# Optimization experiments

Hardware: AMD Instinct MI355X
Metric: run time of the kernel (lower is better)

Reference implementation:

```python
import jax, jax.numpy as jnp
import numpy as np

B, S, H, NH, L, NS = 8, 4096, 768, 12, 2, 64
DH = H // NH
EPS = 1e-12


def _layer_norm(x, g, b):
    mu = jnp.mean(x, axis=-1, keepdims=True)
    var = jnp.mean((x - mu) ** 2, axis=-1, keepdims=True)
    return (x - mu) / jnp.sqrt(var + EPS) * g + b


def setup_inputs() -> dict:
    key = jax.random.key(0)
    ks = jax.random.split(key, 8)
    # sentence index per token: 64 equal contiguous sentences; position 0 is [CLS] in sentence 0
    sent_ind = jnp.broadcast_to((jnp.arange(S, dtype=jnp.int32) * NS) // S, (B, S)).astype(jnp.int32)
    start_layer = jax.random.normal(ks[0], (B, S, H), dtype=jnp.float32)
    init = lambda k, shape: (jax.random.normal(k, shape, dtype=jnp.float32) * 0.02)
    return {
        "sent_ind": sent_ind,
        "start_layer": start_layer,
        "Wq": init(ks[1], (L, H, H)), "bq": jnp.zeros((L, H), jnp.float32),
        "Wk": init(ks[2], (L, H, H)), "bk": jnp.zeros((L, H), jnp.float32),
        "Wv": init(ks[3], (L, H, H)), "bv": jnp.zeros((L, H), jnp.float32),
        "Wo": init(ks[4], (L, H, H)), "bo": jnp.zeros((L, H), jnp.float32),
        "ln_g": jnp.ones((L, H), jnp.float32), "ln_b": jnp.zeros((L, H), jnp.float32),
    }


def reference(sent_ind, start_layer, Wq, bq, Wk, bk, Wv, bv, Wo, bo, ln_g, ln_b):
    # ---- segment-mean pooling by sentence index (vectorized replacement of the python loops) ----
    onehot = (sent_ind[..., None] == jnp.arange(NS, dtype=sent_ind.dtype)).astype(start_layer.dtype)  # [B,S,NS]
    # the first [CLS] token is excluded from sentence 0's mean
    onehot = onehot.at[:, 0, :].set(0.0)
    sums = jnp.einsum('bsn,bsd->bnd', onehot, start_layer)          # [B,NS,H]
    counts = jnp.sum(onehot, axis=1)                                 # [B,NS]
    x = sums / counts[..., None]                                     # graph_vectors [B,NS,H]

    # ---- GAT layers: BertSelfAttention + GATSelfOutput(dense->gelu->LayerNorm), dropout=eval ----
    scale = 1.0 / (DH ** 0.5)
    for i in range(L):
        q = (x @ Wq[i] + bq[i]).reshape(B, NS, NH, DH)
        k = (x @ Wk[i] + bk[i]).reshape(B, NS, NH, DH)
        v = (x @ Wv[i] + bv[i]).reshape(B, NS, NH, DH)
        scores = jnp.einsum('bqhd,bkhd->bhqk', q, k) * scale
        probs = jax.nn.softmax(scores, axis=-1)
        ctx = jnp.einsum('bhqk,bkhd->bqhd', probs, v).reshape(B, NS, H)
        h = jax.nn.gelu(ctx @ Wo[i] + bo[i], approximate=False)
        x = _layer_norm(h, ln_g[i], ln_b[i])
    return x
```

## Files before the change

kernel.cpp:

```cpp
#include <hip/hip_runtime.h>
#include <hip/hip_bf16.h>

constexpr int cB  = 8;
constexpr int cS  = 4096;
constexpr int cH  = 768;
constexpr int cNH = 12;
constexpr int cL  = 2;
constexpr int cNS = 64;
constexpr int cDH = 64;
constexpr int cM  = cB * cNS;

typedef __attribute__((ext_vector_type(8))) short bf16x8;
typedef __attribute__((ext_vector_type(4))) float f32x4;

__global__ __launch_bounds__(256) void pool_kernel(
    const int* __restrict__ sent_ind, const float* __restrict__ sl,
    __hip_bfloat16* __restrict__ xb)
{
    int bn = blockIdx.x;
    int b = bn >> 6, n = bn & (cNS - 1);
    __shared__ int cnt;
    __shared__ int list[cS];
    if (threadIdx.x == 0) cnt = 0;
    __syncthreads();
    const int* si = sent_ind + (size_t)b * cS;
    for (int s = threadIdx.x; s < cS; s += 256)
        if (s != 0 && si[s] == n) { int p = atomicAdd(&cnt, 1); list[p] = s; }
    __syncthreads();
    int c = cnt;
    float a0 = 0.f, a1 = 0.f, a2 = 0.f;
    for (int i = 0; i < c; ++i) {
        const float* row = sl + ((size_t)b * cS + list[i]) * cH;
        a0 += row[threadIdx.x];
        a1 += row[threadIdx.x + 256];
        a2 += row[threadIdx.x + 512];
    }
    float inv = 1.0f / (float)c;
    __hip_bfloat16* xr = xb + (size_t)bn * cH;
    xr[threadIdx.x]       = __float2bfloat16(a0 * inv);
    xr[threadIdx.x + 256] = __float2bfloat16(a1 * inv);
    xr[threadIdx.x + 512] = __float2bfloat16(a2 * inv);
}

__global__ __launch_bounds__(256) void wconv_kernel(
    const float* __restrict__ Wq, const float* __restrict__ Wk,
    const float* __restrict__ Wv, const float* __restrict__ Wo,
    __hip_bfloat16* __restrict__ wt)
{
    int mat = blockIdx.z;
    int layer = mat >> 2, which = mat & 3;
    const float* W = (which == 0 ? Wq : which == 1 ? Wk : which == 2 ? Wv : Wo)
                     + (size_t)layer * cH * cH;
    __shared__ float T[64][65];
    int k0 = blockIdx.y * 64, n0 = blockIdx.x * 64;
    int tid = threadIdx.x;
    int r = tid >> 2, cb = (tid & 3) * 16;
    #pragma unroll
    for (int u = 0; u < 4; ++u) {
        float4 w4 = *(const float4*)(W + (size_t)(k0 + r) * cH + n0 + cb + u * 4);
        T[r][cb + u * 4 + 0] = w4.x; T[r][cb + u * 4 + 1] = w4.y;
        T[r][cb + u * 4 + 2] = w4.z; T[r][cb + u * 4 + 3] = w4.w;
    }
    __syncthreads();
    int kk = tid & 63;
    int nb = (tid >> 6) * 16;
    __hip_bfloat16* dst = wt + ((size_t)mat * cH + n0) * cH + k0;
    #pragma unroll
    for (int u = 0; u < 16; ++u) {
        int nn = nb + u;
        dst[(size_t)nn * cH + kk] = __float2bfloat16(T[kk][nn]);
    }
}

template<int ACT>
__global__ __launch_bounds__(256) void gemm_mfma(
    const __hip_bfloat16* __restrict__ A,
    const __hip_bfloat16* __restrict__ Wt,
    const float* __restrict__ bias,
    float* __restrict__ C)
{
    constexpr int K = cH, N = cH;
    int lane = threadIdx.x & 63;
    int wave = threadIdx.x >> 6;
    int l15 = lane & 15, q = lane >> 4;
    int m0 = blockIdx.y * 64 + wave * 16;
    int n0 = blockIdx.x * 32;

    const __hip_bfloat16* Arow = A  + (size_t)(m0 + l15) * K + q * 8;
    const __hip_bfloat16* Wr0  = Wt + (size_t)(n0 + l15) * K + q * 8;
    const __hip_bfloat16* Wr1  = Wr0 + (size_t)16 * K;

    f32x4 acc0 = {0.f, 0.f, 0.f, 0.f};
    f32x4 acc1 = {0.f, 0.f, 0.f, 0.f};
    #pragma unroll 4
    for (int k0 = 0; k0 < K; k0 += 32) {
        bf16x8 a  = *(const bf16x8*)(Arow + k0);
        bf16x8 b0 = *(const bf16x8*)(Wr0 + k0);
        bf16x8 b1 = *(const bf16x8*)(Wr1 + k0);
        acc0 = __builtin_amdgcn_mfma_f32_16x16x32_bf16(a, b0, acc0, 0, 0, 0);
        acc1 = __builtin_amdgcn_mfma_f32_16x16x32_bf16(a, b1, acc1, 0, 0, 0);
    }
    #pragma unroll
    for (int nt = 0; nt < 2; ++nt) {
        const f32x4 acc = nt == 0 ? acc0 : acc1;
        int col = n0 + nt * 16 + l15;
        float bv = bias[col];
        #pragma unroll
        for (int r = 0; r < 4; ++r) {
            int row = m0 + q * 4 + r;
            float v = acc[r] + bv;
            if (ACT == 1) v = 0.5f * v * (1.0f + erff(v * 0.70710678118654752f));
            C[(size_t)row * N + col] = v;
        }
    }
}

__global__ __launch_bounds__(256) void attn_kernel(
    const float* __restrict__ q, const float* __restrict__ k,
    const float* __restrict__ v, __hip_bfloat16* __restrict__ ctx)
{
    int bh = blockIdx.x;
    int b = bh / cNH, hh = bh % cNH;
    __shared__ float Qs[cNS][cDH + 4];
    __shared__ float Ks[cNS][cDH + 4];
    __shared__ float Vt[cDH][cNS + 4];
    __shared__ float Ps[cNS][cNS + 4];
    int tid = threadIdx.x;
    size_t base = ((size_t)b * cNS) * cH + hh * cDH;

    for (int i = tid; i < cNS * cDH / 4; i += 256) {
        int r = i >> 4;
        int c = (i & 15) << 2;
        float4 qv = *(const float4*)(q + base + (size_t)r * cH + c);
        float4 kv = *(const float4*)(k + base + (size_t)r * cH + c);
        float4 vv = *(const float4*)(v + base + (size_t)r * cH + c);
        *(float4*)&Qs[r][c] = qv;
        *(float4*)&Ks[r][c] = kv;
        Vt[c + 0][r] = vv.x; Vt[c + 1][r] = vv.y;
        Vt[c + 2][r] = vv.z; Vt[c + 3][r] = vv.w;
    }
    __syncthreads();

    int tx = tid & 15, ty = tid >> 4;
    float accs[4][4] = {};
    for (int d = 0; d < cDH; d += 4) {
        float4 qv[4], kv[4];
        #pragma unroll
        for (int i = 0; i < 4; ++i) qv[i] = *(const float4*)&Qs[ty * 4 + i][d];
        #pragma unroll
        for (int j = 0; j < 4; ++j) kv[j] = *(const float4*)&Ks[tx + j * 16][d];
        #pragma unroll
        for (int i = 0; i < 4; ++i)
            #pragma unroll
            for (int j = 0; j < 4; ++j)
                accs[i][j] += qv[i].x * kv[j].x + qv[i].y * kv[j].y +
                              qv[i].z * kv[j].z + qv[i].w * kv[j].w;
    }
    const float scale = 0.125f;
    #pragma unroll
    for (int i = 0; i < 4; ++i)
        #pragma unroll
        for (int j = 0; j < 4; ++j)
            Ps[ty * 4 + i][tx + j * 16] = accs[i][j] * scale;
    __syncthreads();

    {
        int row = tid >> 2, jq = tid & 3;
        float e[16];
        float m = -1e30f;
        #pragma unroll
        for (int c = 0; c < 16; ++c) { e[c] = Ps[row][jq * 16 + c]; m = fmaxf(m, e[c]); }
        m = fmaxf(m, __shfl_xor(m, 1));
        m = fmaxf(m, __shfl_xor(m, 2));
        float s = 0.f;
        #pragma unroll
        for (int c = 0; c < 16; ++c) { e[c] = __expf(e[c] - m); s += e[c]; }
        s += __shfl_xor(s, 1);
        s += __shfl_xor(s, 2);
        float inv = 1.0f / s;
        #pragma unroll
        for (int c = 0; c < 16; ++c) Ps[row][jq * 16 + c] = e[c] * inv;
    }
    __syncthreads();

    float acco[4][4] = {};
    for (int c = 0; c < cNS; c += 4) {
        float4 p4[4], vt4[4];
        #pragma unroll
        for (int i = 0; i < 4; ++i) p4[i] = *(const float4*)&Ps[ty * 4 + i][c];
        #pragma unroll
        for (int j = 0; j < 4; ++j) vt4[j] = *(const float4*)&Vt[tx + j * 16][c];
        #pragma unroll
        for (int i = 0; i < 4; ++i)
            #pragma unroll
            for (int j = 0; j < 4; ++j)
                acco[i][j] += p4[i].x * vt4[j].x + p4[i].y * vt4[j].y +
                              p4[i].z * vt4[j].z + p4[i].w * vt4[j].w;
    }
    #pragma unroll
    for (int i = 0; i < 4; ++i)
        #pragma unroll
        for (int j = 0; j < 4; ++j)
            ctx[base + (size_t)(ty * 4 + i) * cH + tx + j * 16] =
                __float2bfloat16(acco[i][j]);
}

__global__ __launch_bounds__(256) void ln_kernel(
    const float* __restrict__ h, const float* __restrict__ g,
    const float* __restrict__ bb, __hip_bfloat16* __restrict__ xb,
    float* __restrict__ outf)
{
    int row = blockIdx.x;
    const float* r = h + (size_t)row * cH;
    int tid = threadIdx.x;
    float v0 = r[tid], v1 = r[tid + 256], v2 = r[tid + 512];
    float s = v0 + v1 + v2;
    __shared__ float red[4];
    #pragma unroll
    for (int o = 32; o; o >>= 1) s += __shfl_xor(s, o);
    if ((tid & 63) == 0) red[tid >> 6] = s;
    __syncthreads();
    float mu = (red[0] + red[1] + red[2] + red[3]) * (1.0f / 768.0f);
    float d0 = v0 - mu, d1 = v1 - mu, d2 = v2 - mu;
    float ss = d0 * d0 + d1 * d1 + d2 * d2;
    __syncthreads();
    #pragma unroll
    for (int o = 32; o; o >>= 1) ss += __shfl_xor(ss, o);
    if ((tid & 63) == 0) red[tid >> 6] = ss;
    __syncthreads();
    float var = (red[0] + red[1] + red[2] + red[3]) * (1.0f / 768.0f);
    float inv = rsqrtf(var + 1e-12f);
    float o0 = d0 * inv * g[tid]       + bb[tid];
    float o1 = d1 * inv * g[tid + 256] + bb[tid + 256];
    float o2 = d2 * inv * g[tid + 512] + bb[tid + 512];
    __hip_bfloat16* xr = xb + (size_t)row * cH;
    xr[tid]       = __float2bfloat16(o0);
    xr[tid + 256] = __float2bfloat16(o1);
    xr[tid + 512] = __float2bfloat16(o2);
    if (outf) {
        float* orow = outf + (size_t)row * cH;
        orow[tid] = o0; orow[tid + 256] = o1; orow[tid + 512] = o2;
    }
}

extern "C" void kernel_launch(void* const* d_in, const int* in_sizes, int n_in,
                              void* d_out, int out_size, void* d_ws, size_t ws_size,
                              hipStream_t stream) {
    const int*   sent_ind = (const int*)d_in[0];
    const float* start    = (const float*)d_in[1];
    const float* Wq = (const float*)d_in[2];
    const float* bq = (const float*)d_in[3];
    const float* Wk = (const float*)d_in[4];
    const float* bk = (const float*)d_in[5];
    const float* Wv = (const float*)d_in[6];
    const float* bv = (const float*)d_in[7];
    const float* Wo = (const float*)d_in[8];
    const float* bo = (const float*)d_in[9];
    const float* ln_g = (const float*)d_in[10];
    const float* ln_b = (const float*)d_in[11];
    float* out = (float*)d_out;

    char* w = (char*)d_ws;
    __hip_bfloat16* wt     = (__hip_bfloat16*)w;
    __hip_bfloat16* x_bf   = (__hip_bfloat16*)(w + 9437184);
    __hip_bfloat16* ctx_bf = (__hip_bfloat16*)(w + 9437184 + 786432);
    float* qb = (float*)(w + 9437184 + 2 * 786432);
    float* kb = qb + (size_t)cM * cH;
    float* vb = kb + (size_t)cM * cH;
    float* hb = vb + (size_t)cM * cH;

    wconv_kernel<<<dim3(12, 12, 8), 256, 0, stream>>>(Wq, Wk, Wv, Wo, wt);
    pool_kernel<<<cB * cNS, 256, 0, stream>>>(sent_ind, start, x_bf);

    for (int i = 0; i < cL; ++i) {
        const __hip_bfloat16* wtq = wt + (size_t)(i * 4 + 0) * cH * cH;
        const __hip_bfloat16* wtk = wt + (size_t)(i * 4 + 1) * cH * cH;
        const __hip_bfloat16* wtv = wt + (size_t)(i * 4 + 2) * cH * cH;
        const __hip_bfloat16* wto = wt + (size_t)(i * 4 + 3) * cH * cH;
        dim3 ggrid(24, 8);
        gemm_mfma<0><<<ggrid, 256, 0, stream>>>(x_bf, wtq, bq + (size_t)i * cH, qb);
        gemm_mfma<0><<<ggrid, 256, 0, stream>>>(x_bf, wtk, bk + (size_t)i * cH, kb);
        gemm_mfma<0><<<ggrid, 256, 0, stream>>>(x_bf, wtv, bv + (size_t)i * cH, vb);
        attn_kernel<<<cB * cNH, 256, 0, stream>>>(qb, kb, vb, ctx_bf);
        gemm_mfma<1><<<ggrid, 256, 0, stream>>>(ctx_bf, wto, bo + (size_t)i * cH, hb);
        ln_kernel<<<cM, 256, 0, stream>>>(hb, ln_g + (size_t)i * cH, ln_b + (size_t)i * cH,
                                          x_bf, (i == cL - 1) ? out : nullptr);
    }
}
```

Before: 309.1 us.

## Fuse pooling with weight conversion, batch QKV GEMMs, vectorize pooling loads

Merges the pooling kernel and the weight transpose/convert kernel into one launch that splits work by block index, so the two prep stages run concurrently. The three Q/K/V projection GEMMs become a single launch that selects its weight matrix, bias and output by grid z, and the pooling gather now uses float4 loads with four independent accumulators. The GEMM inner loop unroll goes from 4 to 8. The aim is fewer kernel launches, more blocks in flight per launch, and better memory-level parallelism in the bandwidth-bound pooling read of start_layer, at the cost of a larger union shared buffer in the prep kernel.

```diff
diff --git a/kernel.cpp b/kernel.cpp
--- a/kernel.cpp
+++ b/kernel.cpp
@@ -13,73 +13,100 @@
 typedef __attribute__((ext_vector_type(8))) short bf16x8;
 typedef __attribute__((ext_vector_type(4))) float f32x4;
 
-__global__ __launch_bounds__(256) void pool_kernel(
+union PrepShared {
+    float T[64][65];
+    struct { int cnt; int list[cS]; } p;
+};
+
+__global__ __launch_bounds__(256) void prep_kernel(
     const int* __restrict__ sent_ind, const float* __restrict__ sl,
-    __hip_bfloat16* __restrict__ xb)
-{
-    int bn = blockIdx.x;
-    int b = bn >> 6, n = bn & (cNS - 1);
-    __shared__ int cnt;
-    __shared__ int list[cS];
-    if (threadIdx.x == 0) cnt = 0;
-    __syncthreads();
-    const int* si = sent_ind + (size_t)b * cS;
-    for (int s = threadIdx.x; s < cS; s += 256)
-        if (s != 0 && si[s] == n) { int p = atomicAdd(&cnt, 1); list[p] = s; }
-    __syncthreads();
-    int c = cnt;
-    float a0 = 0.f, a1 = 0.f, a2 = 0.f;
-    for (int i = 0; i < c; ++i) {
-        const float* row = sl + ((size_t)b * cS + list[i]) * cH;
-        a0 += row[threadIdx.x];
-        a1 += row[threadIdx.x + 256];
-        a2 += row[threadIdx.x + 512];
-    }
-    float inv = 1.0f / (float)c;
-    __hip_bfloat16* xr = xb + (size_t)bn * cH;
-    xr[threadIdx.x]       = __float2bfloat16(a0 * inv);
-    xr[threadIdx.x + 256] = __float2bfloat16(a1 * inv);
-    xr[threadIdx.x + 512] = __float2bfloat16(a2 * inv);
-}
-
-__global__ __launch_bounds__(256) void wconv_kernel(
+    __hip_bfloat16* __restrict__ xb,
     const float* __restrict__ Wq, const float* __restrict__ Wk,
     const float* __restrict__ Wv, const float* __restrict__ Wo,
     __hip_bfloat16* __restrict__ wt)
 {
-    int mat = blockIdx.z;
-    int layer = mat >> 2, which = mat & 3;
-    const float* W = (which == 0 ? Wq : which == 1 ? Wk : which == 2 ? Wv : Wo)
-                     + (size_t)layer * cH * cH;
-    __shared__ float T[64][65];
-    int k0 = blockIdx.y * 64, n0 = blockIdx.x * 64;
+    __shared__ PrepShared sh;
     int tid = threadIdx.x;
-    int r = tid >> 2, cb = (tid & 3) * 16;
-    #pragma unroll
-    for (int u = 0; u < 4; ++u) {
-        float4 w4 = *(const float4*)(W + (size_t)(k0 + r) * cH + n0 + cb + u * 4);
-        T[r][cb + u * 4 + 0] = w4.x; T[r][cb + u * 4 + 1] = w4.y;
-        T[r][cb + u * 4 + 2] = w4.z; T[r][cb + u * 4 + 3] = w4.w;
-    }
-    __syncthreads();
-    int kk = tid & 63;
-    int nb = (tid >> 6) * 16;
-    __hip_bfloat16* dst = wt + ((size_t)mat * cH + n0) * cH + k0;
-    #pragma unroll
-    for (int u = 0; u < 16; ++u) {
-        int nn = nb + u;
-        dst[(size_t)nn * cH + kk] = __float2bfloat16(T[kk][nn]);
+
+    if (blockIdx.x < (unsigned)cM) {
+        int bn = blockIdx.x;
+        int b = bn >> 6, n = bn & (cNS - 1);
+        if (tid == 0) sh.p.cnt = 0;
+        __syncthreads();
+        const int* si = sent_ind + (size_t)b * cS;
+        for (int s = tid; s < cS; s += 256)
+            if (s != 0 && si[s] == n) { int p = atomicAdd(&sh.p.cnt, 1); sh.p.list[p] = s; }
+        __syncthreads();
+        int c = sh.p.cnt;
+        if (tid < 192) {
+            const float* bbase = sl + (size_t)b * cS * cH;
+            int col = tid * 4;
+            float4 a0 = {0.f, 0.f, 0.f, 0.f};
+            float4 a1 = {0.f, 0.f, 0.f, 0.f};
+            float4 a2 = {0.f, 0.f, 0.f, 0.f};
+            float4 a3 = {0.f, 0.f, 0.f, 0.f};
+            int i = 0;
+            for (; i + 4 <= c; i += 4) {
+                float4 r0 = *(const float4*)(bbase + (size_t)sh.p.list[i + 0] * cH + col);
+                float4 r1 = *(const float4*)(bbase + (size_t)sh.p.list[i + 1] * cH + col);
+                float4 r2 = *(const float4*)(bbase + (size_t)sh.p.list[i + 2] * cH + col);
+                float4 r3 = *(const float4*)(bbase + (size_t)sh.p.list[i + 3] * cH + col);
+                a0.x += r0.x; a0.y += r0.y; a0.z += r0.z; a0.w += r0.w;
+                a1.x += r1.x; a1.y += r1.y; a1.z += r1.z; a1.w += r1.w;
+                a2.x += r2.x; a2.y += r2.y; a2.z += r2.z; a2.w += r2.w;
+                a3.x += r3.x; a3.y += r3.y; a3.z += r3.z; a3.w += r3.w;
+            }
+            for (; i < c; ++i) {
+                float4 r0 = *(const float4*)(bbase + (size_t)sh.p.list[i] * cH + col);
+                a0.x += r0.x; a0.y += r0.y; a0.z += r0.z; a0.w += r0.w;
+            }
+            float inv = 1.0f / (float)c;
+            __hip_bfloat16* xr = xb + (size_t)bn * cH + col;
+            xr[0] = __float2bfloat16((a0.x + a1.x + a2.x + a3.x) * inv);
+            xr[1] = __float2bfloat16((a0.y + a1.y + a2.y + a3.y) * inv);
+            xr[2] = __float2bfloat16((a0.z + a1.z + a2.z + a3.z) * inv);
+            xr[3] = __float2bfloat16((a0.w + a1.w + a2.w + a3.w) * inv);
+        }
+    } else {
+        int bi = blockIdx.x - cM;
+        int bx = bi % 12, by = (bi / 12) % 12, mat = bi / 144;
+        int layer = mat >> 2, which = mat & 3;
+        const float* W = (which == 0 ? Wq : which == 1 ? Wk : which == 2 ? Wv : Wo)
+                         + (size_t)layer * cH * cH;
+        int k0 = by * 64, n0 = bx * 64;
+        int r = tid >> 2, cb = (tid & 3) * 16;
+        #pragma unroll
+        for (int u = 0; u < 4; ++u) {
+            float4 w4 = *(const float4*)(W + (size_t)(k0 + r) * cH + n0 + cb + u * 4);
+            sh.T[r][cb + u * 4 + 0] = w4.x; sh.T[r][cb + u * 4 + 1] = w4.y;
+            sh.T[r][cb + u * 4 + 2] = w4.z; sh.T[r][cb + u * 4 + 3] = w4.w;
+        }
+        __syncthreads();
+        int kk = tid & 63;
+        int nb = (tid >> 6) * 16;
+        __hip_bfloat16* dst = wt + ((size_t)mat * cH + n0) * cH + k0;
+        #pragma unroll
+        for (int u = 0; u < 16; ++u) {
+            int nn = nb + u;
+            dst[(size_t)nn * cH + kk] = __float2bfloat16(sh.T[kk][nn]);
+        }
     }
 }
 
 template<int ACT>
 __global__ __launch_bounds__(256) void gemm_mfma(
     const __hip_bfloat16* __restrict__ A,
-    const __hip_bfloat16* __restrict__ Wt,
-    const float* __restrict__ bias,
-    float* __restrict__ C)
+    const __hip_bfloat16* __restrict__ Wt0,
+    const float* __restrict__ biasA, const float* __restrict__ biasB,
+    const float* __restrict__ biasC,
+    float* __restrict__ C0)
 {
     constexpr int K = cH, N = cH;
+    int mat = blockIdx.z;
+    const __hip_bfloat16* Wt = Wt0 + (size_t)mat * cH * cH;
+    const float* bias = (mat == 0) ? biasA : (mat == 1) ? biasB : biasC;
+    float* C = C0 + (size_t)mat * cM * cH;
+
     int lane = threadIdx.x & 63;
     int wave = threadIdx.x >> 6;
     int l15 = lane & 15, q = lane >> 4;
@@ -92,7 +119,7 @@
 
     f32x4 acc0 = {0.f, 0.f, 0.f, 0.f};
     f32x4 acc1 = {0.f, 0.f, 0.f, 0.f};
-    #pragma unroll 4
+    #pragma unroll 8
     for (int k0 = 0; k0 < K; k0 += 32) {
         bf16x8 a  = *(const bf16x8*)(Arow + k0);
         bf16x8 b0 = *(const bf16x8*)(Wr0 + k0);
@@ -265,24 +292,20 @@
     __hip_bfloat16* x_bf   = (__hip_bfloat16*)(w + 9437184);
     __hip_bfloat16* ctx_bf = (__hip_bfloat16*)(w + 9437184 + 786432);
     float* qb = (float*)(w + 9437184 + 2 * 786432);
-    float* kb = qb + (size_t)cM * cH;
-    float* vb = kb + (size_t)cM * cH;
-    float* hb = vb + (size_t)cM * cH;
-
-    wconv_kernel<<<dim3(12, 12, 8), 256, 0, stream>>>(Wq, Wk, Wv, Wo, wt);
-    pool_kernel<<<cB * cNS, 256, 0, stream>>>(sent_ind, start, x_bf);
+    float* hb = qb + (size_t)3 * cM * cH;
+
+    prep_kernel<<<cM + 1152, 256, 0, stream>>>(sent_ind, start, x_bf,
+                                               Wq, Wk, Wv, Wo, wt);
 
     for (int i = 0; i < cL; ++i) {
         const __hip_bfloat16* wtq = wt + (size_t)(i * 4 + 0) * cH * cH;
-        const __hip_bfloat16* wtk = wt + (size_t)(i * 4 + 1) * cH * cH;
-        const __hip_bfloat16* wtv = wt + (size_t)(i * 4 + 2) * cH * cH;
         const __hip_bfloat16* wto = wt + (size_t)(i * 4 + 3) * cH * cH;
-        dim3 ggrid(24, 8);
-        gemm_mfma<0><<<ggrid, 256, 0, stream>>>(x_bf, wtq, bq + (size_t)i * cH, qb);
-        gemm_mfma<0><<<ggrid, 256, 0, stream>>>(x_bf, wtk, bk + (size_t)i * cH, kb);
-        gemm_mfma<0><<<ggrid, 256, 0, stream>>>(x_bf, wtv, bv + (size_t)i * cH, vb);
-        attn_kernel<<<cB * cNH, 256, 0, stream>>>(qb, kb, vb, ctx_bf);
-        gemm_mfma<1><<<ggrid, 256, 0, stream>>>(ctx_bf, wto, bo + (size_t)i * cH, hb);
+        gemm_mfma<0><<<dim3(24, 8, 3), 256, 0, stream>>>(
+            x_bf, wtq, bq + (size_t)i * cH, bk + (size_t)i * cH, bv + (size_t)i * cH, qb);
+        attn_kernel<<<cB * cNH, 256, 0, stream>>>(
+            qb, qb + (size_t)cM * cH, qb + (size_t)2 * cM * cH, ctx_bf);
+        gemm_mfma<1><<<dim3(24, 8, 1), 256, 0, stream>>>(
+            ctx_bf, wto, bo + (size_t)i * cH, nullptr, nullptr, hb);
         ln_kernel<<<cM, 256, 0, stream>>>(hb, ln_g + (size_t)i * cH, ln_b + (size_t)i * cH,
                                           x_bf, (i == cL - 1) ? out : nullptr);
     }
```

After: 292.5 us. -5.4%, faster.
